# Kernel optimization log

Measured on AMD Instinct MI355X. Metric: run time of the kernel, lower is better.

The kernel has to match this reference:

```python
import math
import jax
import jax.numpy as jnp
import numpy as np

LMAX = 6                 # lmax
F8, F2 = 16, 64          # f_out//8, f_out//2 for f_out=128
DIM6 = sum((2 * l + 1) ** 2 for l in range(LMAX + 1))  # 455 = dim of so3_irreps(6)
NA = NB = NG = 16        # SO(3) activation grid (alpha, beta, gamma)
B, T, H, C = 32, 16, 4, 128


def _real_sh(lmax, xyz):
    # real spherical harmonics: (N,3) unit vectors -> (N,(lmax+1)^2), m=-l..l per l
    x, y, z = xyz[:, 0], xyz[:, 1], xyz[:, 2]
    st = np.sqrt(np.clip(1.0 - z * z, 0.0, None))
    phi = np.arctan2(y, x)
    n = xyz.shape[0]
    P = np.zeros((lmax + 1, lmax + 1, n))
    P[0, 0] = 1.0
    for m in range(1, lmax + 1):
        P[m, m] = -(2 * m - 1) * st * P[m - 1, m - 1]
    for m in range(lmax):
        P[m + 1, m] = (2 * m + 1) * z * P[m, m]
    for m in range(lmax + 1):
        for l in range(m + 2, lmax + 1):
            P[l, m] = ((2 * l - 1) * z * P[l - 1, m] - (l + m - 1) * P[l - 2, m]) / (l - m)
    cols = []
    for l in range(lmax + 1):
        for m in range(-l, l + 1):
            am = abs(m)
            K = math.sqrt((2 * l + 1) / (4 * math.pi) * math.factorial(l - am) / math.factorial(l + am))
            if m > 0:
                cols.append(math.sqrt(2.0) * K * np.cos(m * phi) * P[l, m])
            elif m < 0:
                cols.append(math.sqrt(2.0) * K * np.sin(am * phi) * P[l, am])
            else:
                cols.append(K * P[l, 0])
    return np.stack(cols, axis=-1)


def _flat_wigner(lmax, Rs):
    # component-normalized flat real Wigner-D basis: (G,3,3) -> (G, sum_l (2l+1)^2)
    # D_l(R) solved from Y_l(R x) = D_l(R) Y_l(x) by least squares in float64
    rng = np.random.default_rng(0)
    pts = rng.normal(size=(32, 3))
    pts /= np.linalg.norm(pts, axis=1, keepdims=True)
    Y = _real_sh(lmax, pts)                                     # (32,(lmax+1)^2)
    rp = np.einsum('gij,nj->gni', Rs, pts).reshape(-1, 3)
    Yr = _real_sh(lmax, rp).reshape(len(Rs), 32, -1)            # (G,32,(lmax+1)^2)
    blocks = []
    for l in range(lmax + 1):
        d = 2 * l + 1
        o = l * l
        Apinv = np.linalg.pinv(Y[:, o:o + d])                   # (d,32)
        D = np.einsum('kn,gnm->gmk', Apinv, Yr[:, :, o:o + d])  # (G,d,d)
        blocks.append(math.sqrt(d) * D.reshape(len(Rs), d * d))
    return np.concatenate(blocks, axis=-1)


def _rz(a):
    c, s = np.cos(a), np.sin(a)
    z, o = np.zeros_like(a), np.ones_like(a)
    return np.stack([np.stack([c, -s, z], -1), np.stack([s, c, z], -1), np.stack([z, z, o], -1)], -2)


def _ry(a):
    c, s = np.cos(a), np.sin(a)
    z, o = np.zeros_like(a), np.ones_like(a)
    return np.stack([np.stack([c, z, s], -1), np.stack([z, o, z], -1), np.stack([-s, z, c], -1)], -2)


def _so3_grid():
    # ZYZ Euler grid, Gauss-Legendre in beta; rotations (G,3,3) + Haar weights (G,) summing to 1
    nodes, wts = np.polynomial.legendre.leggauss(NB)
    betas = np.arccos(nodes)
    alphas = np.arange(NA) * 2 * np.pi / NA
    gammas = np.arange(NG) * 2 * np.pi / NG
    Aa, Bb, Cg = np.meshgrid(alphas, betas, gammas, indexing='ij')
    Rs = _rz(Aa.ravel()) @ _ry(Bb.ravel()) @ _rz(Cg.ravel())
    w = np.broadcast_to(wts[None, :, None], (NA, NB, NG)).ravel().copy()
    w *= (2 * np.pi / NA) * (2 * np.pi / NG) / (8 * np.pi ** 2)
    return Rs, w


def _ico_rotations():
    # the 60 rotations of the icosahedral group, generated by closure
    phi = (1.0 + 5.0 ** 0.5) / 2.0
    def rot(axis, ang):
        a = np.asarray(axis, dtype=np.float64)
        a = a / np.linalg.norm(a)
        K = np.array([[0.0, -a[2], a[1]], [a[2], 0.0, -a[0]], [-a[1], a[0], 0.0]])
        return np.eye(3) + math.sin(ang) * K + (1.0 - math.cos(ang)) * (K @ K)
    gens = [rot([0.0, 1.0, phi], 2.0 * np.pi / 5.0), rot([0.0, 0.0, 1.0], np.pi)]
    elems = [np.eye(3)]
    seen = {tuple(np.round(np.eye(3), 5).ravel())}
    frontier = list(elems)
    while frontier:
        nxt = []
        for R in frontier:
            for g in gens:
                Q = g @ R
                k = tuple(np.round(Q, 5).ravel())
                if k not in seen:
                    seen.add(k)
                    elems.append(Q)
                    nxt.append(Q)
        frontier = nxt
    return np.stack(elems)


def _equi_linear(xl, wl):
    # e3nn-style per-irrep linear: xl (...,f_in,u,m), wl (f_in,f_out,u,v); fan_in = f_in*u
    fan_in = wl.shape[0] * wl.shape[2]
    return jnp.einsum('...fum,fguv->...gvm', xl, wl) / np.sqrt(fan_in)


def _forward(x, trajectory, w1s, w1v, w2, D_in, D_outw, ico_wigners):
    b, t, _ = trajectory.shape
    # pack '1x0e+3x1e': scalar = traj[...,9], vectors = traj[...,:9]
    s = trajectory[..., 9][..., None, None, None]       # (b,t,f=1,u=1,m=1)
    v = trajectory[..., :9].reshape(b, t, 1, 3, 3)      # (b,t,f=1,u=3,m=3)
    h = jnp.concatenate([_equi_linear(s, w1s).reshape(b, t, F8, 1),
                         _equi_linear(v, w1v).reshape(b, t, F8, 9)], axis=-1)  # (b,t,16,10)
    # SO(3) activation: coeffs -> grid signal -> relu -> coeffs (lmax 1 -> 6)
    sig = jax.nn.relu(jnp.einsum('btci,gi->btcg', h, D_in))
    h = jnp.einsum('btcg,gi->btci', sig, D_outw)        # (b,t,16,455)
    # per-l equivariant linear, f 16 -> 64
    outs = []
    o = 0
    for l in range(LMAX + 1):
        d = 2 * l + 1
        xl = h[..., o:o + d * d].reshape(b, t, F8, d, d)
        outs.append(_equi_linear(xl, w2[l]).reshape(b, t, F2, d * d))
        o += d * d
    traj = jnp.concatenate(outs, axis=-1)               # (b,t,64,455)
    traj = jnp.einsum('bhcj,ij->bhci', traj, ico_wigners)  # sample on ico rotations
    xg = jnp.einsum('bhcj,ij->bhci', x, ico_wigners)
    return xg, traj


def setup_inputs():
    key = jax.random.key(0)
    ks = jax.random.split(key, 11)
    Rs, w = _so3_grid()
    D_in = _flat_wigner(1, Rs).astype(np.float32)                      # (G,10)
    D_outw = (_flat_wigner(LMAX, Rs) * w[:, None]).astype(np.float32)  # (G,455)
    ico = _flat_wigner(LMAX, _ico_rotations()).astype(np.float32)      # (60,455)
    inp = dict(
        x=jax.random.normal(ks[0], (B, H, C, DIM6), jnp.float32),
        trajectory=jax.random.normal(ks[1], (B, T, 10), jnp.float32),
        w1s=jax.random.normal(ks[2], (1, F8, 1, 1), jnp.float32),
        w1v=jax.random.normal(ks[3], (1, F8, 3, 3), jnp.float32),
        D_in=jnp.asarray(D_in),
        D_outw=jnp.asarray(D_outw),
        ico_wigners=jnp.asarray(ico),
    )
    for l in range(LMAX + 1):
        inp['w2_%d' % l] = jax.random.normal(ks[4 + l], (F8, F2, 2 * l + 1, 2 * l + 1), jnp.float32)
    return inp


def reference(x, trajectory, w1s, w1v, w2_0, w2_1, w2_2, w2_3, w2_4, w2_5, w2_6, D_in, D_outw, ico_wigners):
    w2 = [w2_0, w2_1, w2_2, w2_3, w2_4, w2_5, w2_6]
    return _forward(x, trajectory, w1s, w1v, w2, D_in, D_outw, ico_wigners)
```

## Files before the change

kernel.cpp:

```cpp
#include <hip/hip_runtime.h>
#include <math.h>


#define NBT  512
#define F8c  16
#define F2c  64
#define GJ   455
#define GG   4096
#define NICO 60
#define JP   512

typedef short bf16x8 __attribute__((ext_vector_type(8)));
typedef float f32x4  __attribute__((ext_vector_type(4)));
typedef unsigned int u32;
typedef unsigned short ushort;

struct W7 { const float* p[7]; };

__device__ __forceinline__ ushort f2bf(float f) {
  u32 u = __float_as_uint(f);
  return (ushort)((u + 0x7fffu + ((u >> 16) & 1u)) >> 16);
}
__device__ __forceinline__ float bf2f(ushort v) {
  return __uint_as_float(((u32)v) << 16);
}

__device__ __forceinline__ int sel7(int l, int a0, int a1, int a2, int a3,
                                    int a4, int a5, int a6) {
  int r = a6;
  r = (l == 5) ? a5 : r; r = (l == 4) ? a4 : r; r = (l == 3) ? a3 : r;
  r = (l == 2) ? a2 : r; r = (l == 1) ? a1 : r; r = (l == 0) ? a0 : r;
  return r;
}
__device__ __forceinline__ float sel7f(int l, float a0, float a1, float a2,
                                       float a3, float a4, float a5, float a6) {
  float r = a6;
  r = (l == 5) ? a5 : r; r = (l == 4) ? a4 : r; r = (l == 3) ? a3 : r;
  r = (l == 2) ? a2 : r; r = (l == 1) ? a1 : r; r = (l == 0) ? a0 : r;
  return r;
}

__global__ __launch_bounds__(256) void k_pre(const float* __restrict__ traj,
                                             const float* __restrict__ w1s,
                                             const float* __restrict__ w1v,
                                             const float* __restrict__ ico,
                                             const float* __restrict__ Dout,
                                             W7 w2,
                                             float* __restrict__ h,
                                             ushort* __restrict__ icoB,
                                             ushort* __restrict__ icoBx,
                                             ushort* __restrict__ DoutBT,
                                             ushort* __restrict__ Abuf,
                                             ushort* __restrict__ Bbuf) {
  __shared__ float t[64][65];
  int b = blockIdx.x, tid = threadIdx.x;
  if (b < 2240) {
    ((uint4*)Abuf)[b * 256 + tid] = (uint4){0, 0, 0, 0};
  } else if (b < 2752) {
    int b2 = b - 2240;
    int jt = b2 & 7, kt = b2 >> 3;
    int tx = tid & 63, ty = tid >> 6;
    #pragma unroll
    for (int i = 0; i < 16; ++i) {
      int r = i * 4 + ty, j = jt * 64 + tx;
      t[r][tx] = (j < GJ) ? Dout[(size_t)(kt * 64 + r) * GJ + j] : 0.f;
    }
    __syncthreads();
    #pragma unroll
    for (int i = 0; i < 16; ++i) {
      int jl = i * 4 + ty;
      DoutBT[(size_t)(jt * 64 + jl) * GG + kt * 64 + tx] = f2bf(t[tx][jl]);
    }
  } else if (b < 4992) {
    int ee = (b - 2752) * 256 + tid;
    if (ee < 573440) {
      int l = (ee >= 4096) + (ee >= 16384) + (ee >= 57344) + (ee >= 114688) +
              (ee >= 225280) + (ee >= 360448);
      int base = sel7(l, 0, 4096, 16384, 57344, 114688, 225280, 360448);
      int d    = sel7(l, 1, 3, 5, 7, 9, 11, 13);
      int Kp   = sel7(l, 64, 64, 128, 128, 192, 192, 256);
      int local = ee - base;
      int row = local / Kp, kcol = local - row * Kp;
      int g2 = row / d, v = row - g2 * d;
      ushort val = 0;
      if (kcol < 16 * d) {
        int f = kcol / d, u = kcol - f * d;
        const float* wl = w2.p[l];
        float scl = rsqrtf(16.f * (float)d);
        val = f2bf(wl[(((size_t)f * 64 + g2) * d + u) * d + v] * scl);
      }
      Bbuf[ee] = val;
    }
  } else if (b < 5312) {
    int idx = (b - 4992) * 256 + tid;
    if (idx < NBT * 160) {
      int bt = idx / 160, r = idx % 160, c = r / 10, i = r % 10;
      const float* tr = traj + bt * 10;
      float val;
      if (i == 0) {
        val = tr[9] * w1s[c];
      } else {
        int k = i - 1, v = k / 3, m = k % 3;
        float s = 0.f;
        #pragma unroll
        for (int u = 0; u < 3; ++u) s = fmaf(tr[u * 3 + m], w1v[c * 9 + u * 3 + v], s);
        val = s * 0.57735026918962576f;
      }
      h[idx] = val;
    }
  } else if (b < 5440) {
    int e = (b - 5312) * 256 + tid;
    int i = e >> 9, k = e & 511;
    ushort val = 0;
    if (i < NICO && k < GJ) {
      int l = (k >= 1) + (k >= 10) + (k >= 35) + (k >= 84) + (k >= 165) + (k >= 286);
      int o = sel7(l, 0, 1, 10, 35, 84, 165, 286);
      int d = sel7(l, 1, 3, 5, 7, 9, 11, 13);
      float rcpd = sel7f(l, 1.f, 1.f / 3.f, 0.2f, 1.f / 7.f, 1.f / 9.f,
                         1.f / 11.f, 1.f / 13.f);
      int local = k - o;
      int m = (int)(((float)local + 0.5f) * rcpd);
      int v = local - m * d;
      val = f2bf(ico[i * GJ + o + v * d + m]);
    }
    icoB[e] = val;
  } else {
    int e = (b - 5440) * 256 + tid;
    int i = e >> 9, j = e & 511;
    icoBx[e] = (i < NICO && j < GJ) ? f2bf(ico[i * GJ + j]) : (ushort)0;
  }
}

__global__ __launch_bounds__(256) void k_sig(const float* __restrict__ h,
                                             const float* __restrict__ Din,
                                             ushort* __restrict__ sigb) {
  __shared__ float hs[160];
  int tid = threadIdx.x;
  int mb = blockIdx.y;
  int kt = blockIdx.x;
  if (tid < 160) hs[tid] = h[mb * 160 + tid];
  float dr[80];
  const float4* dp = (const float4*)(Din + (size_t)(kt * 2048 + tid * 8) * 10);
  #pragma unroll
  for (int q = 0; q < 20; ++q) {
    float4 v = dp[q];
    dr[q * 4 + 0] = v.x; dr[q * 4 + 1] = v.y; dr[q * 4 + 2] = v.z; dr[q * 4 + 3] = v.w;
  }
  __syncthreads();
  #pragma unroll
  for (int r = 0; r < 16; ++r) {
    float hv[10];
    #pragma unroll
    for (int i = 0; i < 10; ++i) hv[i] = hs[r * 10 + i];
    bf16x8 o;
    #pragma unroll
    for (int j = 0; j < 8; ++j) {
      float s = 0.f;
      #pragma unroll
      for (int i = 0; i < 10; ++i) s = fmaf(hv[i], dr[j * 10 + i], s);
      o[j] = (short)f2bf(fmaxf(s, 0.f));
    }
    *(bf16x8*)&sigb[((size_t)(mb * 16 + r)) * GG + kt * 2048 + tid * 8] = o;
  }
}

__global__ __launch_bounds__(256) void k_mm2s(const ushort* __restrict__ A,
                                              const ushort* __restrict__ Bm,
                                              ushort* __restrict__ part) {
  __shared__ __align__(16) short Asb[2][128 * 64];
  __shared__ __align__(16) short Bsb[2][128 * 64];
  int tid = threadIdx.x;
  int lane = tid & 63, wid = tid >> 6;
  int quad = lane >> 4, lr = lane & 15;
  int wm = wid >> 1, wn = wid & 1;
  int bid = blockIdx.x;
  int mb = bid & 63;
  int split = (bid >> 6) & 1;
  int nb = bid >> 7;
  int k0 = split * 2048;

  const ushort* Ab = A + (size_t)mb * 128 * GG + k0;
  const ushort* Bb = Bm + (size_t)nb * 128 * GG + k0;

  f32x4 acc[4][4];
  #pragma unroll
  for (int a = 0; a < 4; ++a)
    #pragma unroll
    for (int b = 0; b < 4; ++b) acc[a][b] = (f32x4){0.f, 0.f, 0.f, 0.f};

  auto stage = [&](int buf, int kc) {
    #pragma unroll
    for (int it = 0; it < 4; ++it) {
      int s0 = (wid * 4 + it) * 64;
      int s = s0 + lane;
      int r = s >> 3, pp = s & 7, p = pp ^ (r & 7);
      __builtin_amdgcn_global_load_lds(
          (const __attribute__((address_space(1))) u32*)(Ab + (size_t)r * GG + kc + p * 8),
          (__attribute__((address_space(3))) u32*)(&Asb[buf][s0 * 8]), 16, 0, 0);
    }
    #pragma unroll
    for (int it = 0; it < 4; ++it) {
      int s0 = (wid * 4 + it) * 64;
      int s = s0 + lane;
      int r = s >> 3, pp = s & 7, p = pp ^ (r & 7);
      __builtin_amdgcn_global_load_lds(
          (const __attribute__((address_space(1))) u32*)(Bb + (size_t)r * GG + kc + p * 8),
          (__attribute__((address_space(3))) u32*)(&Bsb[buf][s0 * 8]), 16, 0, 0);
    }
  };

  stage(0, 0);
  __syncthreads();
  for (int it = 0; it < 32; ++it) {
    int cur = it & 1;
    if (it < 31) stage(cur ^ 1, (it + 1) * 64);
    #pragma unroll
    for (int ks = 0; ks < 2; ++ks) {
      bf16x8 af[4], bv[4];
      #pragma unroll
      for (int mt = 0; mt < 4; ++mt) {
        int ra = wm * 64 + mt * 16 + lr;
        int v = (ks * 4 + quad) ^ (ra & 7);
        af[mt] = *(const bf16x8*)&Asb[cur][(ra * 8 + v) * 8];
      }
      #pragma unroll
      for (int nt = 0; nt < 4; ++nt) {
        int rb = wn * 64 + nt * 16 + lr;
        int v = (ks * 4 + quad) ^ (rb & 7);
        bv[nt] = *(const bf16x8*)&Bsb[cur][(rb * 8 + v) * 8];
      }
      #pragma unroll
      for (int mt = 0; mt < 4; ++mt)
        #pragma unroll
        for (int nt = 0; nt < 4; ++nt)
          acc[mt][nt] = __builtin_amdgcn_mfma_f32_16x16x32_bf16(af[mt], bv[nt], acc[mt][nt], 0, 0, 0);
    }
    __syncthreads();
  }
  #pragma unroll
  for (int mt = 0; mt < 4; ++mt)
    #pragma unroll
    for (int nt = 0; nt < 4; ++nt) {
      int j = nb * 128 + wn * 64 + nt * 16 + lr;
      #pragma unroll
      for (int r = 0; r < 4; ++r) {
        int m = mb * 128 + wm * 64 + mt * 16 + quad * 4 + r;
        part[((size_t)split * 8192 + m) * 512 + j] = f2bf(acc[mt][nt][r]);
      }
    }
}

__global__ __launch_bounds__(256) void k_red(const ushort* __restrict__ part,
                                             ushort* __restrict__ Abuf) {
  int t = blockIdx.x * 256 + threadIdx.x;
  int e0 = t * 8;
  int m = e0 >> 9, j0 = e0 & 511;
  bf16x8 a0 = *(const bf16x8*)(part + (size_t)m * 512 + j0);
  bf16x8 b0 = *(const bf16x8*)(part + (size_t)(8192 + m) * 512 + j0);
  float s[8];
  #pragma unroll
  for (int i = 0; i < 8; ++i)
    s[i] = bf2f((ushort)a0[i]) + bf2f((ushort)b0[i]);
  int btg = m >> 4, f = m & 15;
  #pragma unroll
  for (int jj = 0; jj < 8; ++jj) {
    int j = j0 + jj;
    if (j < GJ) {
      int l = (j >= 1) + (j >= 10) + (j >= 35) + (j >= 84) + (j >= 165) + (j >= 286);
      int o    = sel7(l, 0, 1, 10, 35, 84, 165, 286);
      int d    = sel7(l, 1, 3, 5, 7, 9, 11, 13);
      int Kp   = sel7(l, 64, 64, 128, 128, 192, 192, 256);
      int Aoff = sel7(l, 0, 32768, 131072, 458752, 917504, 1802240, 2883584);
      float rcpd = sel7f(l, 1.f, 1.f / 3.f, 0.2f, 1.f / 7.f, 1.f / 9.f,
                         1.f / 11.f, 1.f / 13.f);
      int jl = j - o;
      int u = (int)(((float)jl + 0.5f) * rcpd);
      int mB = jl - u * d;
      Abuf[(size_t)Aoff + ((size_t)btg * d + mB) * Kp + f * d + u] = f2bf(s[jj]);
    }
  }
}

__global__ __launch_bounds__(256) void k_mm2f(const ushort* __restrict__ A,
                                              const ushort* __restrict__ Bm,
                                              ushort* __restrict__ Abuf) {
  __shared__ __align__(16) short Asb[2][128 * 64];
  __shared__ __align__(16) short Bsb[2][128 * 64];
  int tid = threadIdx.x;
  int lane = tid & 63, wid = tid >> 6;
  int quad = lane >> 4, lr = lane & 15;
  int wm = wid >> 1, wn = wid & 1;
  int bid = blockIdx.x;
  int mb = bid & 63, nb = bid >> 6;
  f32x4 acc[4][4];
  #pragma unroll
  for (int a = 0; a < 4; ++a)
    #pragma unroll
    for (int b = 0; b < 4; ++b) acc[a][b] = (f32x4){0.f, 0.f, 0.f, 0.f};
  const ushort* Ab = A + (size_t)mb * 128 * GG;
  const ushort* Bb = Bm + (size_t)nb * 128 * GG;
  auto stage = [&](int buf, int kc) {
    #pragma unroll
    for (int it = 0; it < 4; ++it) {
      int s0 = (wid * 4 + it) * 64;
      int s = s0 + lane;
      int r = s >> 3, pp = s & 7, p = pp ^ (r & 7);
      __builtin_amdgcn_global_load_lds(
          (const __attribute__((address_space(1))) u32*)(Ab + (size_t)r * GG + kc + p * 8),
          (__attribute__((address_space(3))) u32*)(&Asb[buf][s0 * 8]), 16, 0, 0);
    }
    #pragma unroll
    for (int it = 0; it < 4; ++it) {
      int s0 = (wid * 4 + it) * 64;
      int s = s0 + lane;
      int r = s >> 3, pp = s & 7, p = pp ^ (r & 7);
      __builtin_amdgcn_global_load_lds(
          (const __attribute__((address_space(1))) u32*)(Bb + (size_t)r * GG + kc + p * 8),
          (__attribute__((address_space(3))) u32*)(&Bsb[buf][s0 * 8]), 16, 0, 0);
    }
  };
  stage(0, 0);
  __syncthreads();
  for (int it = 0; it < 64; ++it) {
    int cur = it & 1;
    if (it < 63) stage(cur ^ 1, (it + 1) * 64);
    #pragma unroll
    for (int ks = 0; ks < 2; ++ks) {
      bf16x8 af[4], bvv[4];
      #pragma unroll
      for (int mt = 0; mt < 4; ++mt) {
        int ra = wm * 64 + mt * 16 + lr;
        int v = (ks * 4 + quad) ^ (ra & 7);
        af[mt] = *(const bf16x8*)&Asb[cur][(ra * 8 + v) * 8];
      }
      #pragma unroll
      for (int nt = 0; nt < 4; ++nt) {
        int rb = wn * 64 + nt * 16 + lr;
        int v = (ks * 4 + quad) ^ (rb & 7);
        bvv[nt] = *(const bf16x8*)&Bsb[cur][(rb * 8 + v) * 8];
      }
      #pragma unroll
      for (int mt = 0; mt < 4; ++mt)
        #pragma unroll
        for (int nt = 0; nt < 4; ++nt)
          acc[mt][nt] = __builtin_amdgcn_mfma_f32_16x16x32_bf16(af[mt], bvv[nt], acc[mt][nt], 0, 0, 0);
    }
    __syncthreads();
  }
  #pragma unroll
  for (int nt = 0; nt < 4; ++nt) {
    int j = nb * 128 + wn * 64 + nt * 16 + lr;
    if (j < GJ) {
      int l = (j >= 1) + (j >= 10) + (j >= 35) + (j >= 84) + (j >= 165) + (j >= 286);
      int o    = sel7(l, 0, 1, 10, 35, 84, 165, 286);
      int d    = sel7(l, 1, 3, 5, 7, 9, 11, 13);
      int Kp   = sel7(l, 64, 64, 128, 128, 192, 192, 256);
      int Aoff = sel7(l, 0, 32768, 131072, 458752, 917504, 1802240, 2883584);
      int jl = j - o;
      float rcpd = 1.0f / (float)d;
      int u = (int)(((float)jl + 0.5f) * rcpd);
      int mB = jl - u * d;
      #pragma unroll
      for (int mt = 0; mt < 4; ++mt)
        #pragma unroll
        for (int r = 0; r < 4; ++r) {
          int m = mb * 128 + wm * 64 + mt * 16 + quad * 4 + r;
          int btg = m >> 4, f = m & 15;
          Abuf[(size_t)Aoff + ((size_t)btg * d + mB) * Kp + f * d + u] =
              f2bf(acc[mt][nt][r]);
        }
    }
  }
}

__global__ __launch_bounds__(256) void k_batchX(const ushort* __restrict__ Abuf,
                                                const ushort* __restrict__ Bbuf,
                                                const float* __restrict__ x,
                                                const ushort* __restrict__ icoBx,
                                                ushort* __restrict__ trajbf,
                                                float* __restrict__ xg) {
  __shared__ __align__(16) short As[128 * 64];
  __shared__ __align__(16) short Bs[128 * 64];
  int bid = blockIdx.x;
  int tid = threadIdx.x;
  int lane = tid & 63, wid = tid >> 6;
  int quad = lane >> 4, lr = lane & 15;
  int wm = wid >> 1, wn = wid & 1;

  if (bid >= 1008) {
    int mtile = bid - 1008;
    f32x4 acc[4][2];
    #pragma unroll
    for (int a = 0; a < 4; ++a)
      #pragma unroll
      for (int b = 0; b < 2; ++b) acc[a][b] = (f32x4){0.f, 0.f, 0.f, 0.f};
    float xn[32];
    auto loadx = [&](int itk) {
      #pragma unroll
      for (int g = 0; g < 4; ++g) {
        int s = g * 256 + tid;
        int r = s >> 3, p8 = s & 7, p = p8 ^ (r & 7);
        const float* xr = x + (size_t)(mtile * 128 + r) * GJ;
        int j0 = itk * 64 + p * 8;
        #pragma unroll
        for (int jj = 0; jj < 8; ++jj) {
          int j = j0 + jj;
          xn[g * 8 + jj] = (j < GJ) ? xr[j] : 0.f;
        }
      }
    };
    auto writex = [&]() {
      #pragma unroll
      for (int g = 0; g < 4; ++g) {
        int s = g * 256 + tid;
        bf16x8 v8;
        #pragma unroll
        for (int jj = 0; jj < 8; ++jj) v8[jj] = (short)f2bf(xn[g * 8 + jj]);
        *(bf16x8*)&As[s * 8] = v8;
      }
    };
    auto stageBx = [&](int kc) {
      #pragma unroll
      for (int it = 0; it < 2; ++it) {
        int s0 = (wid * 2 + it) * 64;
        int s = s0 + lane;
        int r = s >> 3, p8 = s & 7, p = p8 ^ (r & 7);
        const ushort* gb = icoBx + (size_t)r * JP + kc + p * 8;
        __builtin_amdgcn_global_load_lds(
            (const __attribute__((address_space(1))) u32*)gb,
            (__attribute__((address_space(3))) u32*)(Bs + s0 * 8), 16, 0, 0);
      }
    };
    loadx(0); writex(); stageBx(0);
    __syncthreads();
    for (int it = 0; it < 8; ++it) {
      if (it < 7) loadx(it + 1);
      #pragma unroll
      for (int ks = 0; ks < 2; ++ks) {
        bf16x8 af[4], bv[2];
        #pragma unroll
        for (int mt = 0; mt < 4; ++mt) {
          int ra = wm * 64 + mt * 16 + lr;
          int v = (ks * 4 + quad) ^ (ra & 7);
          af[mt] = *(const bf16x8*)&As[(ra * 8 + v) * 8];
        }
        #pragma unroll
        for (int nt = 0; nt < 2; ++nt) {
          int rb = wn * 32 + nt * 16 + lr;
          int v = (ks * 4 + quad) ^ (rb & 7);
          bv[nt] = *(const bf16x8*)&Bs[(rb * 8 + v) * 8];
        }
        #pragma unroll
        for (int mt = 0; mt < 4; ++mt)
          #pragma unroll
          for (int nt = 0; nt < 2; ++nt)
            acc[mt][nt] = __builtin_amdgcn_mfma_f32_16x16x32_bf16(af[mt], bv[nt], acc[mt][nt], 0, 0, 0);
      }
      if (it < 7) {
        __syncthreads();
        writex();
        stageBx((it + 1) * 64);
        __syncthreads();
      }
    }
    #pragma unroll
    for (int mt = 0; mt < 4; ++mt)
      #pragma unroll
      for (int nt = 0; nt < 2; ++nt) {
        int i = wn * 32 + nt * 16 + lr;
        if (i < NICO) {
          #pragma unroll
          for (int r = 0; r < 4; ++r) {
            int row = mtile * 128 + wm * 64 + mt * 16 + quad * 4 + r;
            xg[(size_t)row * NICO + i] = acc[mt][nt][r];
          }
        }
      }
    return;
  }

  f32x4 acc[4][4];
  #pragma unroll
  for (int a = 0; a < 4; ++a)
    #pragma unroll
    for (int b = 0; b < 4; ++b) acc[a][b] = (f32x4){0.f, 0.f, 0.f, 0.f};

  int l = (bid >= 4) + (bid >= 28) + (bid >= 88) + (bid >= 200) +
          (bid >= 380) + (bid >= 644);
  int bbase = sel7(l, 0, 4, 28, 88, 200, 380, 644);
  int d     = sel7(l, 1, 3, 5, 7, 9, 11, 13);
  int Kp    = sel7(l, 64, 64, 128, 128, 192, 192, 256);
  int o     = sel7(l, 0, 1, 10, 35, 84, 165, 286);
  int Aoff  = sel7(l, 0, 32768, 131072, 458752, 917504, 1802240, 2883584);
  int Boff  = sel7(l, 0, 4096, 16384, 57344, 114688, 225280, 360448);
  int ntc   = sel7(l, 1, 2, 3, 4, 5, 6, 7);
  float rcpntc = sel7f(l, 1.f, 0.5f, 1.f / 3.f, 0.25f, 0.2f, 1.f / 6.f, 1.f / 7.f);
  float rcpd   = sel7f(l, 1.f, 1.f / 3.f, 0.2f, 1.f / 7.f, 1.f / 9.f,
                       1.f / 11.f, 1.f / 13.f);
  int t = bid - bbase;
  int mtile = (int)(((float)t + 0.5f) * rcpntc);
  int ntile = t - mtile * ntc;
  int Nl = 64 * d;

  const ushort* Ab = Abuf + Aoff + (size_t)mtile * 128 * Kp;
  const ushort* Bb = Bbuf + Boff + (size_t)ntile * 128 * Kp;

  auto stage = [&](int kc) {
    #pragma unroll
    for (int it = 0; it < 4; ++it) {
      int s0 = (wid * 4 + it) * 64;
      int s = s0 + lane;
      int r = s >> 3, pp = s & 7, p = pp ^ (r & 7);
      __builtin_amdgcn_global_load_lds(
          (const __attribute__((address_space(1))) u32*)(Ab + (size_t)r * Kp + kc + p * 8),
          (__attribute__((address_space(3))) u32*)(As + s0 * 8), 16, 0, 0);
    }
    #pragma unroll
    for (int it = 0; it < 4; ++it) {
      int s0 = (wid * 4 + it) * 64;
      int s = s0 + lane;
      int r = s >> 3, pp = s & 7, p = pp ^ (r & 7);
      __builtin_amdgcn_global_load_lds(
          (const __attribute__((address_space(1))) u32*)(Bb + (size_t)r * Kp + kc + p * 8),
          (__attribute__((address_space(3))) u32*)(Bs + s0 * 8), 16, 0, 0);
    }
  };

  int nIter = Kp >> 6;
  for (int it = 0; it < nIter; ++it) {
    if (it) __syncthreads();
    stage(it * 64);
    __syncthreads();
    #pragma unroll
    for (int ks = 0; ks < 2; ++ks) {
      bf16x8 af[4], bv[4];
      #pragma unroll
      for (int mt = 0; mt < 4; ++mt) {
        int ra = wm * 64 + mt * 16 + lr;
        int v = (ks * 4 + quad) ^ (ra & 7);
        af[mt] = *(const bf16x8*)&As[(ra * 8 + v) * 8];
      }
      #pragma unroll
      for (int nt = 0; nt < 4; ++nt) {
        int rb = wn * 64 + nt * 16 + lr;
        int v = (ks * 4 + quad) ^ (rb & 7);
        bv[nt] = *(const bf16x8*)&Bs[(rb * 8 + v) * 8];
      }
      #pragma unroll
      for (int mt = 0; mt < 4; ++mt)
        #pragma unroll
        for (int nt = 0; nt < 4; ++nt)
          acc[mt][nt] = __builtin_amdgcn_mfma_f32_16x16x32_bf16(af[mt], bv[nt], acc[mt][nt], 0, 0, 0);
    }
  }
  #pragma unroll
  for (int nt = 0; nt < 4; ++nt) {
    int Ncol = ntile * 128 + wn * 64 + nt * 16 + lr;
    if (Ncol < Nl) {
      int g2 = (int)(((float)Ncol + 0.5f) * rcpd);
      int v = Ncol - g2 * d;
      #pragma unroll
      for (int mt = 0; mt < 4; ++mt)
        #pragma unroll
        for (int r = 0; r < 4; ++r) {
          int Mrow = mtile * 128 + wm * 64 + mt * 16 + quad * 4 + r;
          int bt = (int)(((float)Mrow + 0.5f) * rcpd);
          int m = Mrow - bt * d;
          trajbf[(size_t)(bt * 64 + g2) * JP + o + m * d + v] = f2bf(acc[mt][nt][r]);
        }
    }
  }
}

__global__ __launch_bounds__(256) void k_icoT(const ushort* __restrict__ trajbf,
                                              const ushort* __restrict__ icoB,
                                              float* __restrict__ trajo) {
  __shared__ __align__(16) short As[128 * 64];
  __shared__ __align__(16) short Bs[64 * 64];
  int mtile = blockIdx.x;
  int tid = threadIdx.x;
  int lane = tid & 63, wid = tid >> 6;
  int quad = lane >> 4, lr = lane & 15;
  int wm = wid >> 1, wn = wid & 1;
  f32x4 acc[4][2];
  #pragma unroll
  for (int a = 0; a < 4; ++a)
    #pragma unroll
    for (int b = 0; b < 2; ++b) acc[a][b] = (f32x4){0.f, 0.f, 0.f, 0.f};

  auto stage = [&](int kc) {
    #pragma unroll
    for (int it = 0; it < 4; ++it) {
      int s0 = (wid * 4 + it) * 64;
      int s = s0 + lane;
      int r = s >> 3, p8 = s & 7, p = p8 ^ (r & 7);
      const ushort* ga = trajbf + (size_t)(mtile * 128 + r) * JP + kc + p * 8;
      __builtin_amdgcn_global_load_lds(
          (const __attribute__((address_space(1))) u32*)ga,
          (__attribute__((address_space(3))) u32*)(As + s0 * 8), 16, 0, 0);
    }
    #pragma unroll
    for (int it = 0; it < 2; ++it) {
      int s0 = (wid * 2 + it) * 64;
      int s = s0 + lane;
      int r = s >> 3, p8 = s & 7, p = p8 ^ (r & 7);
      const ushort* gb = icoB + (size_t)r * JP + kc + p * 8;
      __builtin_amdgcn_global_load_lds(
          (const __attribute__((address_space(1))) u32*)gb,
          (__attribute__((address_space(3))) u32*)(Bs + s0 * 8), 16, 0, 0);
    }
  };

  for (int it = 0; it < 8; ++it) {
    if (it) __syncthreads();
    stage(it * 64);
    __syncthreads();
    #pragma unroll
    for (int ks = 0; ks < 2; ++ks) {
      bf16x8 af[4], bv[2];
      #pragma unroll
      for (int mt = 0; mt < 4; ++mt) {
        int ra = wm * 64 + mt * 16 + lr;
        int v = (ks * 4 + quad) ^ (ra & 7);
        af[mt] = *(const bf16x8*)&As[(ra * 8 + v) * 8];
      }
      #pragma unroll
      for (int nt = 0; nt < 2; ++nt) {
        int rb = wn * 32 + nt * 16 + lr;
        int v = (ks * 4 + quad) ^ (rb & 7);
        bv[nt] = *(const bf16x8*)&Bs[(rb * 8 + v) * 8];
      }
      #pragma unroll
      for (int mt = 0; mt < 4; ++mt)
        #pragma unroll
        for (int nt = 0; nt < 2; ++nt)
          acc[mt][nt] = __builtin_amdgcn_mfma_f32_16x16x32_bf16(af[mt], bv[nt], acc[mt][nt], 0, 0, 0);
    }
  }
  #pragma unroll
  for (int mt = 0; mt < 4; ++mt)
    #pragma unroll
    for (int nt = 0; nt < 2; ++nt) {
      int i = wn * 32 + nt * 16 + lr;
      if (i < NICO) {
        #pragma unroll
        for (int r = 0; r < 4; ++r) {
          int row = mtile * 128 + wm * 64 + mt * 16 + quad * 4 + r;
          trajo[(size_t)row * NICO + i] = acc[mt][nt][r];
        }
      }
    }
}

extern "C" void kernel_launch(void* const* d_in, const int* in_sizes, int n_in,
                              void* d_out, int out_size, void* d_ws, size_t ws_size,
                              hipStream_t stream) {
  const float *x = nullptr, *traj = nullptr, *w1s = nullptr, *w1v = nullptr;
  const float *Din = nullptr, *Dout = nullptr, *ico = nullptr;
  W7 w2{};
  for (int i = 0; i < n_in; ++i) {
    const float* p = (const float*)d_in[i];
    switch (in_sizes[i]) {
      case 7454720: x = p; break;
      case 5120:    traj = p; break;
      case 16:      w1s = p; break;
      case 144:     w1v = p; break;
      case 40960:   Din = p; break;
      case 1863680: Dout = p; break;
      case 27300:   ico = p; break;
      case 1024:    w2.p[0] = p; break;
      case 9216:    w2.p[1] = p; break;
      case 25600:   w2.p[2] = p; break;
      case 50176:   w2.p[3] = p; break;
      case 82944:   w2.p[4] = p; break;
      case 123904:  w2.p[5] = p; break;
      case 173056:  w2.p[6] = p; break;
      default: break;
    }
  }
  char* wsb = (char*)d_ws;
  float*  h       = (float*)wsb;
  ushort* DoutBT  = (ushort*)(wsb + 327680);
  ushort* icoB    = (ushort*)(wsb + 4521984);
  ushort* icoBx   = (ushort*)(wsb + 4587520);
  ushort* Abuf    = (ushort*)(wsb + 4653056);
  ushort* Bbuf    = (ushort*)(wsb + 13828096);
  ushort* sigb    = (ushort*)(wsb + 14974976);
  ushort* trajbf  = sigb;
  ushort* part    = (ushort*)(wsb + 82083840);
  float* xg    = (float*)d_out;
  float* trajo = (float*)d_out + 983040;

  k_pre<<<dim3(5568), dim3(256), 0, stream>>>(traj, w1s, w1v, ico, Dout, w2,
                                              h, icoB, icoBx, DoutBT, Abuf, Bbuf);
  k_sig<<<dim3(2, 512), dim3(256), 0, stream>>>(h, Din, sigb);
  if (ws_size >= 115638272ULL) {
    k_mm2s<<<dim3(512),  dim3(256), 0, stream>>>(sigb, DoutBT, part);
    k_red <<<dim3(2048), dim3(256), 0, stream>>>(part, Abuf);
  } else {
    k_mm2f<<<dim3(256),  dim3(256), 0, stream>>>(sigb, DoutBT, Abuf);
  }
  k_batchX<<<dim3(1136), dim3(256), 0, stream>>>(Abuf, Bbuf, x, icoBx, trajbf, xg);
  k_icoT  <<<dim3(256),  dim3(256), 0, stream>>>(trajbf, icoB, trajo);
}
```

Before: 236.8 us.

## Fuse activation-grid sigmoid/relu generation into the split-K GEMM via MFMA

The separate k_sig pass, which materialized a 8192x4096 bf16 activation matrix in global memory, is replaced by computing each 128x64 A tile on the fly inside the GEMM kernel. Each tile is produced with a small MFMA of h (K=10, padded to 32) against a padded bf16 copy of D_in, followed by relu. The padded D_in copy is added to the preprocessing kernel. This removes a large global write and read, but the GEMM loses its double-buffered prefetch, adds extra barriers per K step, and h is now rounded to bf16 before the small product.

```diff
diff --git a/kernel.cpp b/kernel.cpp
--- a/kernel.cpp
+++ b/kernel.cpp
@@ -12,6 +12,7 @@
 
 typedef short bf16x8 __attribute__((ext_vector_type(8)));
 typedef float f32x4  __attribute__((ext_vector_type(4)));
+typedef unsigned short u16x4 __attribute__((ext_vector_type(4)));
 typedef unsigned int u32;
 typedef unsigned short ushort;
 
@@ -45,13 +46,15 @@
                                              const float* __restrict__ w1v,
                                              const float* __restrict__ ico,
                                              const float* __restrict__ Dout,
+                                             const float* __restrict__ Din,
                                              W7 w2,
                                              float* __restrict__ h,
                                              ushort* __restrict__ icoB,
                                              ushort* __restrict__ icoBx,
                                              ushort* __restrict__ DoutBT,
                                              ushort* __restrict__ Abuf,
-                                             ushort* __restrict__ Bbuf) {
+                                             ushort* __restrict__ Bbuf,
+                                             ushort* __restrict__ DinB) {
   __shared__ float t[64][65];
   int b = blockIdx.x, tid = threadIdx.x;
   if (b < 2240) {
@@ -124,10 +127,16 @@
       val = f2bf(ico[i * GJ + o + v * d + m]);
     }
     icoB[e] = val;
-  } else {
+  } else if (b < 5568) {
     int e = (b - 5440) * 256 + tid;
     int i = e >> 9, j = e & 511;
     icoBx[e] = (i < NICO && j < GJ) ? f2bf(ico[i * GJ + j]) : (ushort)0;
+  } else {
+    int g = (b - 5568) * 256 + tid;
+    const float* dr = Din + (size_t)g * 10;
+    #pragma unroll
+    for (int k = 0; k < 32; ++k)
+      DinB[(size_t)g * 32 + k] = (k < 10) ? f2bf(dr[k]) : (ushort)0;
   }
 }
 
@@ -164,11 +173,13 @@
   }
 }
 
-__global__ __launch_bounds__(256) void k_mm2s(const ushort* __restrict__ A,
+__global__ __launch_bounds__(256) void k_fsig(const float* __restrict__ hg,
+                                              const ushort* __restrict__ DinB,
                                               const ushort* __restrict__ Bm,
                                               ushort* __restrict__ part) {
-  __shared__ __align__(16) short Asb[2][128 * 64];
-  __shared__ __align__(16) short Bsb[2][128 * 64];
+  __shared__ __align__(16) short As[128 * 72];
+  __shared__ __align__(16) short Bs[128 * 64];
+  __shared__ __align__(16) short Ds[64 * 40];
   int tid = threadIdx.x;
   int lane = tid & 63, wid = tid >> 6;
   int quad = lane >> 4, lr = lane & 15;
@@ -179,55 +190,74 @@
   int nb = bid >> 7;
   int k0 = split * 2048;
 
-  const ushort* Ab = A + (size_t)mb * 128 * GG + k0;
   const ushort* Bb = Bm + (size_t)nb * 128 * GG + k0;
 
+  bf16x8 haf[2];
+  #pragma unroll
+  for (int t = 0; t < 2; ++t) {
+    int m = mb * 128 + wid * 32 + t * 16 + lr;
+    const float* hr = hg + (size_t)m * 10;
+    bf16x8 v;
+    #pragma unroll
+    for (int j = 0; j < 8; ++j) {
+      int k = quad * 8 + j;
+      v[j] = (k < 10) ? (short)f2bf(hr[k]) : (short)0;
+    }
+    haf[t] = v;
+  }
+
   f32x4 acc[4][4];
   #pragma unroll
   for (int a = 0; a < 4; ++a)
     #pragma unroll
     for (int b = 0; b < 4; ++b) acc[a][b] = (f32x4){0.f, 0.f, 0.f, 0.f};
-
-  auto stage = [&](int buf, int kc) {
-    #pragma unroll
-    for (int it = 0; it < 4; ++it) {
-      int s0 = (wid * 4 + it) * 64;
+  const f32x4 zf = {0.f, 0.f, 0.f, 0.f};
+
+  for (int it = 0; it < 32; ++it) {
+    if (it) __syncthreads();
+    #pragma unroll
+    for (int s4 = 0; s4 < 4; ++s4) {
+      int s0 = (wid * 4 + s4) * 64;
       int s = s0 + lane;
       int r = s >> 3, pp = s & 7, p = pp ^ (r & 7);
       __builtin_amdgcn_global_load_lds(
-          (const __attribute__((address_space(1))) u32*)(Ab + (size_t)r * GG + kc + p * 8),
-          (__attribute__((address_space(3))) u32*)(&Asb[buf][s0 * 8]), 16, 0, 0);
-    }
-    #pragma unroll
-    for (int it = 0; it < 4; ++it) {
-      int s0 = (wid * 4 + it) * 64;
-      int s = s0 + lane;
-      int r = s >> 3, pp = s & 7, p = pp ^ (r & 7);
-      __builtin_amdgcn_global_load_lds(
-          (const __attribute__((address_space(1))) u32*)(Bb + (size_t)r * GG + kc + p * 8),
-          (__attribute__((address_space(3))) u32*)(&Bsb[buf][s0 * 8]), 16, 0, 0);
-    }
-  };
-
-  stage(0, 0);
-  __syncthreads();
-  for (int it = 0; it < 32; ++it) {
-    int cur = it & 1;
-    if (it < 31) stage(cur ^ 1, (it + 1) * 64);
+          (const __attribute__((address_space(1))) u32*)(Bb + (size_t)r * GG + it * 64 + p * 8),
+          (__attribute__((address_space(3))) u32*)(Bs + s0 * 8), 16, 0, 0);
+    }
+    {
+      int kr = tid >> 2, kq = tid & 3;
+      bf16x8 dv = *(const bf16x8*)&DinB[(size_t)(k0 + it * 64 + kr) * 32 + kq * 8];
+      *(bf16x8*)&Ds[kr * 40 + kq * 8] = dv;
+    }
+    __syncthreads();
+    bf16x8 dinf[4];
+    #pragma unroll
+    for (int gt = 0; gt < 4; ++gt)
+      dinf[gt] = *(const bf16x8*)&Ds[(gt * 16 + lr) * 40 + quad * 8];
+    #pragma unroll
+    for (int t = 0; t < 2; ++t) {
+      int m = wid * 32 + t * 16 + lr;
+      #pragma unroll
+      for (int gt = 0; gt < 4; ++gt) {
+        f32x4 sg = __builtin_amdgcn_mfma_f32_16x16x32_bf16(dinf[gt], haf[t], zf, 0, 0, 0);
+        u16x4 o;
+        #pragma unroll
+        for (int r = 0; r < 4; ++r) o[r] = f2bf(fmaxf(sg[r], 0.f));
+        *(u16x4*)&As[m * 72 + gt * 16 + quad * 4] = o;
+      }
+    }
+    __syncthreads();
     #pragma unroll
     for (int ks = 0; ks < 2; ++ks) {
       bf16x8 af[4], bv[4];
       #pragma unroll
-      for (int mt = 0; mt < 4; ++mt) {
-        int ra = wm * 64 + mt * 16 + lr;
-        int v = (ks * 4 + quad) ^ (ra & 7);
-        af[mt] = *(const bf16x8*)&Asb[cur][(ra * 8 + v) * 8];
-      }
+      for (int mt = 0; mt < 4; ++mt)
+        af[mt] = *(const bf16x8*)&As[(wm * 64 + mt * 16 + lr) * 72 + ks * 32 + quad * 8];
       #pragma unroll
       for (int nt = 0; nt < 4; ++nt) {
         int rb = wn * 64 + nt * 16 + lr;
         int v = (ks * 4 + quad) ^ (rb & 7);
-        bv[nt] = *(const bf16x8*)&Bsb[cur][(rb * 8 + v) * 8];
+        bv[nt] = *(const bf16x8*)&Bs[(rb * 8 + v) * 8];
       }
       #pragma unroll
       for (int mt = 0; mt < 4; ++mt)
@@ -235,7 +265,6 @@
         for (int nt = 0; nt < 4; ++nt)
           acc[mt][nt] = __builtin_amdgcn_mfma_f32_16x16x32_bf16(af[mt], bv[nt], acc[mt][nt], 0, 0, 0);
     }
-    __syncthreads();
   }
   #pragma unroll
   for (int mt = 0; mt < 4; ++mt)
@@ -688,16 +717,18 @@
   ushort* sigb    = (ushort*)(wsb + 14974976);
   ushort* trajbf  = sigb;
   ushort* part    = (ushort*)(wsb + 82083840);
+  ushort* DinB    = (ushort*)(wsb + 98861056);
   float* xg    = (float*)d_out;
   float* trajo = (float*)d_out + 983040;
 
-  k_pre<<<dim3(5568), dim3(256), 0, stream>>>(traj, w1s, w1v, ico, Dout, w2,
-                                              h, icoB, icoBx, DoutBT, Abuf, Bbuf);
-  k_sig<<<dim3(2, 512), dim3(256), 0, stream>>>(h, Din, sigb);
+  k_pre<<<dim3(5584), dim3(256), 0, stream>>>(traj, w1s, w1v, ico, Dout, Din,
+                                              w2, h, icoB, icoBx, DoutBT, Abuf,
+                                              Bbuf, DinB);
   if (ws_size >= 115638272ULL) {
-    k_mm2s<<<dim3(512),  dim3(256), 0, stream>>>(sigb, DoutBT, part);
+    k_fsig<<<dim3(512),  dim3(256), 0, stream>>>(h, DinB, DoutBT, part);
     k_red <<<dim3(2048), dim3(256), 0, stream>>>(part, Abuf);
   } else {
+    k_sig<<<dim3(2, 512), dim3(256), 0, stream>>>(h, Din, sigb);
     k_mm2f<<<dim3(256),  dim3(256), 0, stream>>>(sigb, DoutBT, Abuf);
   }
   k_batchX<<<dim3(1136), dim3(256), 0, stream>>>(Abuf, Bbuf, x, icoBx, trajbf, xg);
```

Measured after the change: 234.5 us. No clear change (-1.0%).
